# Kernel tuning notes

Hardware: AMD Instinct MI355X
Metric: run time of the kernel (lower is better)

## Reference

```python
import jax, jax.numpy as jnp
import numpy as np

B, N, H = 32, 256, 1024
HEADS, NHID = 8, 128
NCLS = 7
BAND = 24
ALPHA = 0.2          # GAT leaky-relu slope
NEG = -9e15          # masked-attention fill, as in pyGAT


def setup_inputs() -> dict:
    key = jax.random.key(0)
    ks = jax.random.split(key, 16)
    def nrm(k, shp, s=0.02):
        return jax.random.normal(k, shp, dtype=jnp.float32) * s
    hidden_cls = jax.random.normal(ks[0], (B, N, H), dtype=jnp.float32)
    hidden_emo = jax.random.normal(ks[1], (B, N, H), dtype=jnp.float32)
    # causal band cliques, diagonal included (GAT uses clique - eye)
    t = jnp.arange(N)
    band = ((t[None, :] <= t[:, None]) & (t[None, :] > t[:, None] - BAND)).astype(jnp.float32)
    clique = jnp.broadcast_to(band, (B, N, N))
    labels = jax.random.randint(ks[2], (B, N), 0, NCLS)
    pooler_W = nrm(ks[3], (H, H)); pooler_b = jnp.zeros((H,), jnp.float32)
    gat_W = nrm(ks[4], (HEADS, H, NHID))
    gat_a1 = nrm(ks[5], (HEADS, NHID)); gat_a2 = nrm(ks[6], (HEADS, NHID))
    out_W = nrm(ks[7], (H, H))            # heads*nhid == H -> nclass=H
    out_a1 = nrm(ks[8], (H,)); out_a2 = nrm(ks[9], (H,))
    lin1_W = nrm(ks[10], (H, H)); lin1_b = jnp.zeros((H,), jnp.float32)
    lin0_W = nrm(ks[11], (2 * H, H)); lin0_b = jnp.zeros((H,), jnp.float32)
    cls_W = nrm(ks[12], (H, NCLS)); cls_b = jnp.zeros((NCLS,), jnp.float32)
    A = jax.random.uniform(ks[13], (NCLS, NCLS), dtype=jnp.float32) + 0.1
    hmm_A = A / A.sum(axis=1, keepdims=True)   # row-stochastic transition matrix
    return dict(hidden_cls=hidden_cls, hidden_emo=hidden_emo, clique=clique,
                labels=labels, pooler_W=pooler_W, pooler_b=pooler_b,
                gat_W=gat_W, gat_a1=gat_a1, gat_a2=gat_a2,
                out_W=out_W, out_a1=out_a1, out_a2=out_a2,
                lin1_W=lin1_W, lin1_b=lin1_b, lin0_W=lin0_W, lin0_b=lin0_b,
                cls_W=cls_W, cls_b=cls_b, hmm_A=hmm_A)


def _lrelu(x):
    return jnp.where(x > 0, x, ALPHA * x)


def reference(hidden_cls, hidden_emo, clique, labels, pooler_W, pooler_b,
              gat_W, gat_a1, gat_a2, out_W, out_a1, out_a2,
              lin1_W, lin1_b, lin0_W, lin0_b, cls_W, cls_b, hmm_A):
    # PoolerAll: dense + tanh on all token states (dropout = identity in eval)
    fea_cls = jnp.tanh(hidden_cls @ pooler_W + pooler_b)   # [B,N,H] (CLS per utt)
    fea_emo = jnp.tanh(hidden_emo @ pooler_W + pooler_b)   # [B,N,H] (mask tok per utt)

    eyeN = jnp.eye(N, dtype=clique.dtype)
    adjm = (clique - eyeN) > 0                             # [B,N,N] GAT adjacency

    def gat_one(x, am):                                    # x [N,H], am [N,N]
        Wh = jnp.einsum('nf,hfd->hnd', x, gat_W)           # [heads,N,nhid]
        e = _lrelu(jnp.einsum('hnd,hd->hn', Wh, gat_a1)[:, :, None]
                   + jnp.einsum('hnd,hd->hn', Wh, gat_a2)[:, None, :])
        att = jax.nn.softmax(jnp.where(am[None], e, NEG), axis=-1)
        h1 = jax.nn.elu(jnp.einsum('hnm,hmd->hnd', att, Wh))
        h1 = jnp.transpose(h1, (1, 0, 2)).reshape(N, HEADS * NHID)
        Wh2 = h1 @ out_W                                   # out attention layer (concat=False)
        e2 = _lrelu((Wh2 @ out_a1)[:, None] + (Wh2 @ out_a2)[None, :])
        h2 = jax.nn.softmax(jnp.where(am, e2, NEG), axis=-1) @ Wh2
        return jax.nn.elu(h2)                              # [N,H]

    gat_out = jax.vmap(gat_one)(fea_cls, adjm)             # [B,N,H]
    # row 0 replaced by (dropout of) fea_cls row 0, as in the original
    g = jnp.concatenate([fea_cls[:, :1], gat_out[:, 1:]], axis=1)
    g = jnp.concatenate([fea_cls, g @ lin1_W + lin1_b], axis=-1) @ lin0_W + lin0_b
    log_gat = jax.nn.softmax(g @ cls_W + cls_b, axis=-1)   # [B,N,NCLS] (probs)

    # HMM emission probs hmm_B(fea) = softmax(classifier(fea))
    Bprob = jax.nn.softmax(fea_emo @ cls_W + cls_b, axis=-1)  # [B,N,NCLS]
    P0 = jnp.full((NCLS,), 1.0 / NCLS, dtype=jnp.float32)
    AT = hmm_A.T

    def hmm_row(Bp, mrow):                                 # Bp [N,NCLS], mrow [N]
        def step(carry, xs):
            p, started = carry
            bt, m = xs
            p_init = P0 * bt; p_init = p_init / p_init.sum()
            p_tr = (AT @ p) * bt; p_tr = p_tr / p_tr.sum()
            p_new = jnp.where(started, p_tr, p_init)
            valid = m > 0.5
            return (jnp.where(valid, p_new, p), started | valid), None
        (p, _), _ = jax.lax.scan(step, (P0, jnp.asarray(False)), (Bp, mrow))
        return p                                           # final filtered posterior

    log_hmm = jax.vmap(lambda Bp, M: jax.vmap(lambda mr: hmm_row(Bp, mr))(M))(Bprob, clique)

    logits = jnp.log((log_gat + log_hmm) * 0.5).reshape(B * N, NCLS)
    lab = labels.reshape(B * N)
    mask = lab >= 0
    picked = jnp.take_along_axis(logits, jnp.where(mask, lab, 0)[:, None], axis=1)[:, 0]
    loss = -(jnp.where(mask, picked, 0.0).sum() / jnp.maximum(mask.sum(), 1).astype(jnp.float32))
    return loss, logits
```

## Files before the change

### kernel.cpp

```cpp
#include <hip/hip_runtime.h>
#include <hip/hip_bf16.h>
#include <math.h>

typedef __hip_bfloat16 bf16;
typedef __attribute__((ext_vector_type(8))) short short8;
typedef __attribute__((ext_vector_type(4))) float float4v;

static constexpr int Bb = 32, Nn = 256, Hh = 1024, HEADS = 8, NHID = 128, NCLS = 7, BAND = 24;
static constexpr int M = Bb * Nn;
static constexpr float ALPHA = 0.2f;
static constexpr long INEL = (long)M * Hh;

__device__ __forceinline__ float tof(bf16 x) { return __bfloat162float(x); }
__device__ __forceinline__ bf16 tob(float x) { return __float2bfloat16(x); }
__device__ __forceinline__ unsigned short f2bits(float x) {
    bf16 h = __float2bfloat16(x);
    return *(unsigned short*)&h;
}
__device__ __forceinline__ float bits2f(unsigned short u) {
    unsigned v = ((unsigned)u) << 16;
    float f;
    __builtin_memcpy(&f, &v, 4);
    return f;
}

__device__ __forceinline__ void gload16(const void* g, void* l) {
    __builtin_amdgcn_global_load_lds(
        (const __attribute__((address_space(1))) void*)g,
        (__attribute__((address_space(3))) void*)l, 16, 0, 0);
}

static constexpr long OFF_PWT  = 0;
static constexpr long OFF_PB   = 1048576;
static constexpr long OFF_WCT  = 1049600;
static constexpr long OFF_GA1  = 2098176;
static constexpr long OFF_GA2  = 2099200;
static constexpr long OFF_OWT  = 2100224;
static constexpr long OFF_OA1  = 3148800;
static constexpr long OFF_OA2  = 3149824;
static constexpr long OFF_L1WT = 3150848;
static constexpr long OFF_L1B  = 4199424;
static constexpr long OFF_L0WT = 4200448;
static constexpr long OFF_L0B  = 6297600;
static constexpr long OFF_CWT  = 6298624;
static constexpr long OFF_CB   = 6305792;
static constexpr long OFF_HA   = 6305799;
static constexpr long W_TOTAL  = 6305848;

__global__ void probe_k(const void* __restrict__ p, int* __restrict__ flag) {
    int t = threadIdx.x;
    int bad = 0;
    for (int i = t; i < 4096; i += 256) {
        float v = tof(((const bf16*)p)[i]);
        if (!(fabsf(v) < 1e4f)) bad = 1;
    }
    __shared__ int sb[256];
    sb[t] = bad; __syncthreads();
    for (int s = 128; s; s >>= 1) { if (t < s) sb[t] |= sb[t + s]; __syncthreads(); }
    if (t == 0) *flag = sb[0] ? 0 : 1;
}

__device__ __forceinline__ float ldany(const void* p, long i, int isb) {
    return isb ? tof(((const bf16*)p)[i]) : ((const float*)p)[i];
}

__global__ void convert_k(const int* __restrict__ flagp,
                          const void* pW, const void* pb, const void* gW,
                          const void* ga1, const void* ga2, const void* oW,
                          const void* oa1, const void* oa2, const void* l1W,
                          const void* l1b, const void* l0W, const void* l0b,
                          const void* cW, const void* cb, const void* hA,
                          bf16* __restrict__ dst) {
    long idx = (long)blockIdx.x * 256 + threadIdx.x;
    if (idx >= W_TOTAL) return;
    int isb = *flagp;
    const void* src; long si;
    if      (idx < OFF_PB)   { long l = idx;            long n = l >> 10, k = l & 1023;
                               src = pW;  si = k * 1024 + n; }
    else if (idx < OFF_WCT)  { src = pb;  si = idx - OFF_PB; }
    else if (idx < OFF_GA1)  { long l = idx - OFF_WCT;  long n = l >> 10, f = l & 1023;
                               long h = n >> 7, d = n & 127;
                               src = gW;  si = h * 131072 + f * 128 + d; }
    else if (idx < OFF_GA2)  { src = ga1; si = idx - OFF_GA1; }
    else if (idx < OFF_OWT)  { src = ga2; si = idx - OFF_GA2; }
    else if (idx < OFF_OA1)  { long l = idx - OFF_OWT;  long n = l >> 10, k = l & 1023;
                               src = oW;  si = k * 1024 + n; }
    else if (idx < OFF_OA2)  { src = oa1; si = idx - OFF_OA1; }
    else if (idx < OFF_L1WT) { src = oa2; si = idx - OFF_OA2; }
    else if (idx < OFF_L1B)  { long l = idx - OFF_L1WT; long n = l >> 10, k = l & 1023;
                               src = l1W; si = k * 1024 + n; }
    else if (idx < OFF_L0WT) { src = l1b; si = idx - OFF_L1B; }
    else if (idx < OFF_L0B)  { long l = idx - OFF_L0WT; long n = l >> 11, k = l & 2047;
                               src = l0W; si = k * 1024 + n; }
    else if (idx < OFF_CWT)  { src = l0b; si = idx - OFF_L0B; }
    else if (idx < OFF_CB)   { long l = idx - OFF_CWT;  long c = l >> 10, k = l & 1023;
                               src = cW;  si = k * 7 + c; }
    else if (idx < OFF_HA)   { src = cb;  si = idx - OFF_CB; }
    else                     { src = hA;  si = idx - OFF_HA; }
    dst[idx] = tob(ldany(src, si, isb));
}

__global__ void convin_k(const int* __restrict__ flagp, const void* __restrict__ s0,
                         const void* __restrict__ s1, bf16* __restrict__ d0,
                         bf16* __restrict__ d1) {
    const int isb = *flagp;
    long i = ((long)blockIdx.x * 256 + threadIdx.x) * 8;
    const void* s; bf16* d; long off;
    if (i < INEL) { s = s0; d = d0; off = i; }
    else          { s = s1; d = d1; off = i - INEL; }
    if (isb) {
        *(int4*)(d + off) = *(const int4*)((const bf16*)s + off);
    } else {
        const float* f = (const float*)s + off;
        unsigned short tmp[8];
        #pragma unroll
        for (int q = 0; q < 8; ++q) tmp[q] = f2bits(f[q]);
        *(int4*)(d + off) = *(int4*)tmp;
    }
}

static constexpr int BUF_USHORT = 384 * 32;

template <int ACT>
__device__ __forceinline__ void gemm_pipe_core(
    const bf16* __restrict__ A0, const bf16* __restrict__ A1, int ksw,
    int strideA, const bf16* __restrict__ Bt, int strideB,
    const bf16* __restrict__ bias, bf16* __restrict__ Cout,
    int Nc, int K, int bm, int bn, unsigned short* lds) {
    const int tid = threadIdx.x;
    const int lane = tid & 63;
    const int wave = tid >> 6;
    const int wm = (wave >> 1) * 128;
    const int wn = (wave & 1) * 64;
    const int l15 = lane & 15, quad = lane >> 4;
    const int csw = ((lane & 3) ^ ((lane >> 2) & 3) ^ (lane >> 4)) * 8;
    const int sc8 = (quad ^ (l15 & 3) ^ (l15 >> 2)) * 8;

    long aoff[4], boff[2];
    #pragma unroll
    for (int o = 0; o < 4; ++o)
        aoff[o] = (long)(bm + wave * 64 + o * 16 + (lane >> 2)) * strideA + csw;
    #pragma unroll
    for (int o = 0; o < 2; ++o)
        boff[o] = (long)(bn + wave * 32 + o * 16 + (lane >> 2)) * strideB + csw;
    const int aDst = wave * 64 * 32;
    const int bDst = (256 + wave * 32) * 32;

    const int nt = K / 32;
    float4v acc[8][4];
    #pragma unroll
    for (int i = 0; i < 8; ++i)
        #pragma unroll
        for (int j = 0; j < 4; ++j) acc[i][j] = (float4v){0.f, 0.f, 0.f, 0.f};

    auto stage = [&](int ts, int bsel) {
        unsigned short* buf = lds + bsel * BUF_USHORT;
        int ksub = ts * 32;
        const bf16* Ap = A0; int ka = ksub;
        if (ksub >= ksw) { Ap = A1; ka = ksub - ksw; }
        #pragma unroll
        for (int o = 0; o < 4; ++o)
            gload16(Ap + aoff[o] + ka, buf + aDst + o * 512);
        #pragma unroll
        for (int o = 0; o < 2; ++o)
            gload16(Bt + boff[o] + ksub, buf + bDst + o * 512);
    };

    stage(0, 0);
    stage(1, 1);
    int cur = 0, nxt = 2;
    for (int t = 0; t < nt; ++t) {
        if (t < nt - 1) asm volatile("s_waitcnt vmcnt(6)" ::: "memory");
        else            asm volatile("s_waitcnt vmcnt(0)" ::: "memory");
        __builtin_amdgcn_s_barrier();
        asm volatile("" ::: "memory");
        if (t + 2 < nt) stage(t + 2, nxt);
        const unsigned short* bufc = lds + cur * BUF_USHORT;
        short8 af[8], bfr[4];
        #pragma unroll
        for (int j = 0; j < 4; ++j)
            bfr[j] = *(const short8*)(bufc + (256 + wn + j * 16 + l15) * 32 + sc8);
        #pragma unroll
        for (int i = 0; i < 8; ++i)
            af[i] = *(const short8*)(bufc + (wm + i * 16 + l15) * 32 + sc8);
        __builtin_amdgcn_s_setprio(1);
        #pragma unroll
        for (int i = 0; i < 8; ++i)
            #pragma unroll
            for (int j = 0; j < 4; ++j)
                acc[i][j] = __builtin_amdgcn_mfma_f32_16x16x32_bf16(bfr[j], af[i], acc[i][j], 0, 0, 0);
        __builtin_amdgcn_s_setprio(0);
        asm volatile("" ::: "memory");
        cur = cur == 2 ? 0 : cur + 1;
        nxt = nxt == 2 ? 0 : nxt + 1;
    }

    #pragma unroll
    for (int j = 0; j < 4; ++j) {
        int gn = bn + wn + j * 16 + quad * 4;
        float bj[4] = {0.f, 0.f, 0.f, 0.f};
        if (bias) {
            #pragma unroll
            for (int r = 0; r < 4; ++r) bj[r] = tof(bias[gn + r]);
        }
        #pragma unroll
        for (int i = 0; i < 8; ++i) {
            int gm = bm + wm + i * 16 + l15;
            float v0 = acc[i][j][0] + bj[0], v1 = acc[i][j][1] + bj[1];
            float v2 = acc[i][j][2] + bj[2], v3 = acc[i][j][3] + bj[3];
            if (ACT == 1) { v0 = tanhf(v0); v1 = tanhf(v1); v2 = tanhf(v2); v3 = tanhf(v3); }
            uint2 u;
            u.x = (unsigned)f2bits(v0) | ((unsigned)f2bits(v1) << 16);
            u.y = (unsigned)f2bits(v2) | ((unsigned)f2bits(v3) << 16);
            *(uint2*)(Cout + (long)gm * Nc + gn) = u;
        }
    }
}

template <int ACT>
__global__ __launch_bounds__(256, 2) void gemm_pipe_k(const bf16* __restrict__ A,
                                                      const bf16* __restrict__ Bt,
                                                      const bf16* __restrict__ bias,
                                                      bf16* __restrict__ Cout,
                                                      int Nc, int K) {
    __shared__ __align__(16) unsigned short lds[3 * BUF_USHORT];
    gemm_pipe_core<ACT>(A, A, K, K, Bt, K, bias, Cout, Nc, K,
                        blockIdx.x * 256, blockIdx.y * 128, lds);
}

__global__ __launch_bounds__(256, 2) void gemmP_pipe_k(const bf16* __restrict__ A0,
                                                       const bf16* __restrict__ A1,
                                                       const bf16* __restrict__ Bt,
                                                       const bf16* __restrict__ bias,
                                                       bf16* __restrict__ C0,
                                                       bf16* __restrict__ C1) {
    __shared__ __align__(16) unsigned short lds[3 * BUF_USHORT];
    const bf16* A = blockIdx.z ? A1 : A0;
    bf16* C = blockIdx.z ? C1 : C0;
    gemm_pipe_core<1>(A, A, Hh, Hh, Bt, Hh, bias, C, Hh, Hh,
                      blockIdx.x * 256, blockIdx.y * 128, lds);
}

__global__ __launch_bounds__(256, 2) void gemm2_pipe_k(const bf16* __restrict__ A0,
                                                       const bf16* __restrict__ A2,
                                                       const bf16* __restrict__ Bt,
                                                       const bf16* __restrict__ bias,
                                                       bf16* __restrict__ Cout) {
    __shared__ __align__(16) unsigned short lds[3 * BUF_USHORT];
    gemm_pipe_core<0>(A0, A2, 1024, 1024, Bt, 2048, bias, Cout, 1024, 2048,
                      blockIdx.x * 256, blockIdx.y * 128, lds);
}

__global__ __launch_bounds__(256) void att1f_k(const bf16* __restrict__ Wh,
                                               const bf16* __restrict__ ga1,
                                               const bf16* __restrict__ ga2,
                                               bf16* __restrict__ h1) {
    __shared__ unsigned short S[152][128];
    __shared__ float f1s[152], f2s[152];
    __shared__ float att[128][25];
    const int bx = blockIdx.x;
    const int b = bx >> 4, h = (bx >> 1) & 7, half = bx & 1;
    const int nbase = half * 128;
    const int mstart = half ? (nbase - (BAND - 1)) : 0;
    const int mcount = half ? (256 - mstart) : 128;
    const int t = threadIdx.x;
    const int c = t & 15;

    float av1[8], av2[8];
    {
        union { int4 v; unsigned short us[8]; } u1, u2;
        u1.v = *(const int4*)(ga1 + h * 128 + c * 8);
        u2.v = *(const int4*)(ga2 + h * 128 + c * 8);
        #pragma unroll
        for (int qq = 0; qq < 8; ++qq) { av1[qq] = bits2f(u1.us[qq]); av2[qq] = bits2f(u2.us[qq]); }
    }

    const int iters = (mcount * 16 + 255) >> 8;
    for (int i = 0; i < iters; ++i) {
        int li = i * 256 + t;
        int mr = li >> 4;
        if (mr < mcount) {
            long ga = (long)(b * 256 + mstart + mr) * 1024 + h * 128 + c * 8;
            union { int4 v; unsigned short us[8]; } u;
            u.v = *(const int4*)(Wh + ga);
            float p1 = 0.f, p2 = 0.f;
            #pragma unroll
            for (int qq = 0; qq < 8; ++qq) {
                float f = bits2f(u.us[qq]);
                p1 += f * av1[qq]; p2 += f * av2[qq];
            }
            *(int4*)&S[mr][c * 8] = u.v;
            #pragma unroll
            for (int mask = 1; mask < 16; mask <<= 1) {
                p1 += __shfl_xor(p1, mask);
                p2 += __shfl_xor(p2, mask);
            }
            if (c == 0) { f1s[mr] = p1; f2s[mr] = p2; }
        }
    }
    __syncthreads();

    if (t < 128) {
        int n = nbase + t;
        if (n > 0) {
            int cnt = n < (BAND - 1) ? n : (BAND - 1);
            int m0 = n - cnt;
            float f1n = f1s[n - mstart];
            float e[BAND - 1];
            float mx = -1e30f;
            for (int i = 0; i < cnt; ++i) {
                float v = f1n + f2s[m0 + i - mstart];
                v = v > 0.f ? v : ALPHA * v;
                e[i] = v; mx = fmaxf(mx, v);
            }
            float ss = 0.f;
            for (int i = 0; i < cnt; ++i) { e[i] = __expf(e[i] - mx); ss += e[i]; }
            float inv = 1.0f / ss;
            for (int i = 0; i < cnt; ++i) att[t][i] = e[i] * inv;
        }
    }
    __syncthreads();

    const int wave = t >> 6, lane = t & 63;
    for (int ln = wave; ln < 128; ln += 4) {
        int n = nbase + ln;
        if (n == 0) continue;
        int cnt = n < (BAND - 1) ? n : (BAND - 1);
        int mr0 = n - cnt - mstart;
        float s0 = 0.f, s1 = 0.f;
        for (int i = 0; i < cnt; ++i) {
            float a = att[ln][i];
            unsigned u = *(const unsigned*)&S[mr0 + i][lane * 2];
            s0 += a * bits2f((unsigned short)(u & 0xffff));
            s1 += a * bits2f((unsigned short)(u >> 16));
        }
        s0 = s0 > 0.f ? s0 : expm1f(s0);
        s1 = s1 > 0.f ? s1 : expm1f(s1);
        unsigned out = (unsigned)f2bits(s0) | ((unsigned)f2bits(s1) << 16);
        *(unsigned*)(h1 + (long)(b * 256 + n) * 1024 + h * 128 + lane * 2) = out;
    }
}

__global__ void mean1_k(const bf16* __restrict__ Wh, bf16* __restrict__ h1) {
    int bh = blockIdx.x;
    int h = bh & 7, b = bh >> 3;
    int lane = threadIdx.x;
    float s0 = 0.f, s1 = 0.f;
    long base = (long)(b * 256) * 1024 + h * 128 + lane * 2;
    for (int m = 0; m < 256; ++m) {
        unsigned u = *(const unsigned*)(Wh + base + (long)m * 1024);
        s0 += bits2f((unsigned short)(u & 0xffff));
        s1 += bits2f((unsigned short)(u >> 16));
    }
    s0 *= (1.0f / 256.0f); s1 *= (1.0f / 256.0f);
    s0 = s0 > 0.f ? s0 : expm1f(s0);
    s1 = s1 > 0.f ? s1 : expm1f(s1);
    unsigned out = (unsigned)f2bits(s0) | ((unsigned)f2bits(s1) << 16);
    *(unsigned*)(h1 + base) = out;
}

__global__ void f12b_k(const bf16* __restrict__ Wh2, const bf16* __restrict__ a1,
                       const bf16* __restrict__ a2, float* __restrict__ f1b,
                       float* __restrict__ f2b) {
    int idx = blockIdx.x;
    int lane = threadIdx.x;
    const bf16* row = Wh2 + (long)idx * 1024 + lane * 16;
    float s1 = 0.f, s2 = 0.f;
    #pragma unroll
    for (int half = 0; half < 2; ++half) {
        union { int4 v; unsigned short us[8]; } x, w1, w2;
        x.v  = *(const int4*)(row + half * 8);
        w1.v = *(const int4*)(a1 + lane * 16 + half * 8);
        w2.v = *(const int4*)(a2 + lane * 16 + half * 8);
        #pragma unroll
        for (int q = 0; q < 8; ++q) {
            float f = bits2f(x.us[q]);
            s1 += f * bits2f(w1.us[q]);
            s2 += f * bits2f(w2.us[q]);
        }
    }
    #pragma unroll
    for (int off = 32; off; off >>= 1) {
        s1 += __shfl_down(s1, off);
        s2 += __shfl_down(s2, off);
    }
    if (lane == 0) { f1b[idx] = s1; f2b[idx] = s2; }
}

__global__ __launch_bounds__(256) void att2f_k(const bf16* __restrict__ Wh2,
                                               const float* __restrict__ f1b,
                                               const float* __restrict__ f2b,
                                               bf16* __restrict__ g) {
    __shared__ unsigned short S[152][128];
    __shared__ float att[128][25];
    const int bx = blockIdx.x;
    const int b = bx >> 4, half = (bx >> 3) & 1, jt = bx & 7;
    const int nbase = half * 128;
    const int mstart = half ? (nbase - (BAND - 1)) : 0;
    const int mcount = half ? (256 - mstart) : 128;
    const int t = threadIdx.x;
    const int c = t & 15;

    const int iters = (mcount * 16 + 255) >> 8;
    for (int i = 0; i < iters; ++i) {
        int li = i * 256 + t;
        int mr = li >> 4;
        if (mr < mcount) {
            long ga = (long)(b * 256 + mstart + mr) * 1024 + jt * 128 + c * 8;
            *(int4*)&S[mr][c * 8] = *(const int4*)(Wh2 + ga);
        }
    }
    __syncthreads();

    if (t < 128) {
        int n = nbase + t;
        if (n > 0) {
            int cnt = n < (BAND - 1) ? n : (BAND - 1);
            int m0 = n - cnt;
            float f1n = f1b[b * 256 + n];
            float e[BAND - 1];
            float mx = -1e30f;
            for (int i = 0; i < cnt; ++i) {
                float v = f1n + f2b[b * 256 + m0 + i];
                v = v > 0.f ? v : ALPHA * v;
                e[i] = v; mx = fmaxf(mx, v);
            }
            float ss = 0.f;
            for (int i = 0; i < cnt; ++i) { e[i] = __expf(e[i] - mx); ss += e[i]; }
            float inv = 1.0f / ss;
            for (int i = 0; i < cnt; ++i) att[t][i] = e[i] * inv;
        }
    }
    __syncthreads();

    const int wave = t >> 6, lane = t & 63;
    for (int ln = wave; ln < 128; ln += 4) {
        int n = nbase + ln;
        if (n == 0) continue;
        int cnt = n < (BAND - 1) ? n : (BAND - 1);
        int mr0 = n - cnt - mstart;
        float s0 = 0.f, s1 = 0.f;
        for (int i = 0; i < cnt; ++i) {
            float a = att[ln][i];
            unsigned u = *(const unsigned*)&S[mr0 + i][lane * 2];
            s0 += a * bits2f((unsigned short)(u & 0xffff));
            s1 += a * bits2f((unsigned short)(u >> 16));
        }
        s0 = s0 > 0.f ? s0 : expm1f(s0);
        s1 = s1 > 0.f ? s1 : expm1f(s1);
        unsigned out = (unsigned)f2bits(s0) | ((unsigned)f2bits(s1) << 16);
        *(unsigned*)(g + (long)(b * 256 + n) * 1024 + jt * 128 + lane * 2) = out;
    }
}

__global__ void g_row0_k(const bf16* __restrict__ fea_cls, bf16* __restrict__ g) {
    int b = blockIdx.x;
    int t = threadIdx.x;
    long base = (long)(b * 256) * 1024 + t * 8;
    *(int4*)(g + base) = *(const int4*)(fea_cls + base);
}

__global__ void cls7_k(const bf16* __restrict__ X, const bf16* __restrict__ Wt,
                       const bf16* __restrict__ b, float* __restrict__ out, int K) {
    int row = blockIdx.x;
    int lane = threadIdx.x;
    float xv[16];
    {
        const bf16* x = X + (long)row * K + lane * 16;
        union { int4 v; unsigned short us[8]; } u0, u1;
        u0.v = *(const int4*)x; u1.v = *(const int4*)(x + 8);
        #pragma unroll
        for (int q = 0; q < 8; ++q) { xv[q] = bits2f(u0.us[q]); xv[q + 8] = bits2f(u1.us[q]); }
    }
    float acc[NCLS];
    #pragma unroll
    for (int cc = 0; cc < NCLS; ++cc) {
        const bf16* wr = Wt + (long)cc * K + lane * 16;
        union { int4 v; unsigned short us[8]; } w0, w1;
        w0.v = *(const int4*)wr; w1.v = *(const int4*)(wr + 8);
        float s = 0.f;
        #pragma unroll
        for (int q = 0; q < 8; ++q) {
            s += xv[q] * bits2f(w0.us[q]);
            s += xv[q + 8] * bits2f(w1.us[q]);
        }
        acc[cc] = s;
    }
    #pragma unroll
    for (int cc = 0; cc < NCLS; ++cc)
        #pragma unroll
        for (int off = 32; off; off >>= 1) acc[cc] += __shfl_down(acc[cc], off);
    if (lane == 0) {
        float mx = -1e30f;
        #pragma unroll
        for (int cc = 0; cc < NCLS; ++cc) { acc[cc] += tof(b[cc]); mx = fmaxf(mx, acc[cc]); }
        float s = 0.f;
        #pragma unroll
        for (int cc = 0; cc < NCLS; ++cc) { acc[cc] = expf(acc[cc] - mx); s += acc[cc]; }
        float inv = 1.0f / s;
        #pragma unroll
        for (int cc = 0; cc < NCLS; ++cc) out[(long)row * NCLS + cc] = acc[cc] * inv;
    }
}

__global__ void hmm_k(const float* __restrict__ Bprob, const bf16* __restrict__ hmm_A,
                      float* __restrict__ out) {
    __shared__ float AT[NCLS][NCLS];
    int t = threadIdx.x;
    if (t < NCLS * NCLS) {
        int i = t / NCLS, j = t % NCLS;
        AT[i][j] = tof(hmm_A[j * NCLS + i]);
    }
    __syncthreads();
    int idx = blockIdx.x * blockDim.x + t;
    int n = idx & 255, b = idx >> 8;
    int t0 = n - (BAND - 1) > 0 ? n - (BAND - 1) : 0;
    const float* Bp = Bprob + (long)(b * 256) * NCLS;
    float p[NCLS];
    float s = 0.f;
    #pragma unroll
    for (int cc = 0; cc < NCLS; ++cc) { p[cc] = Bp[t0 * NCLS + cc]; s += p[cc]; }
    float inv = 1.0f / s;
    #pragma unroll
    for (int cc = 0; cc < NCLS; ++cc) p[cc] *= inv;
    for (int tt = t0 + 1; tt <= n; ++tt) {
        float q[NCLS]; float ss = 0.f;
        #pragma unroll
        for (int i = 0; i < NCLS; ++i) {
            float a = 0.f;
            #pragma unroll
            for (int j = 0; j < NCLS; ++j) a += AT[i][j] * p[j];
            a *= Bp[tt * NCLS + i];
            q[i] = a; ss += a;
        }
        float iv = 1.0f / ss;
        #pragma unroll
        for (int i = 0; i < NCLS; ++i) p[i] = q[i] * iv;
    }
    #pragma unroll
    for (int cc = 0; cc < NCLS; ++cc) out[(long)idx * NCLS + cc] = p[cc];
}

__global__ void zero_k(float* p) { *p = 0.f; }

__global__ void final_k(const float* __restrict__ lg, const float* __restrict__ lh,
                        const int* __restrict__ labels, void* __restrict__ out,
                        float* __restrict__ loss_acc, const int* __restrict__ flagp) {
    int idx = blockIdx.x * blockDim.x + threadIdx.x;
    const int isb = *flagp;
    float lo[NCLS];
    int lab = labels[idx];
    #pragma unroll
    for (int c = 0; c < NCLS; ++c) {
        float v = logf(0.5f * (lg[(long)idx * NCLS + c] + lh[(long)idx * NCLS + c]));
        lo[c] = v;
        long o = 1 + (long)idx * NCLS + c;
        if (isb) ((bf16*)out)[o] = tob(v);
        else     ((float*)out)[o] = v;
    }
    float picked = lo[lab];
    __shared__ float red[256];
    red[threadIdx.x] = picked;
    __syncthreads();
    for (int s = 128; s; s >>= 1) {
        if (threadIdx.x < s) red[threadIdx.x] += red[threadIdx.x + s];
        __syncthreads();
    }
    if (threadIdx.x == 0) atomicAdd(loss_acc, red[0]);
}

__global__ void loss_k(const float* __restrict__ acc, void* __restrict__ out,
                       const int* __restrict__ flagp) {
    float v = -acc[0] / (float)(Bb * Nn);
    if (*flagp) ((bf16*)out)[0] = tob(v);
    else        ((float*)out)[0] = v;
}

extern "C" void kernel_launch(void* const* d_in, const int* in_sizes, int n_in,
                              void* d_out, int out_size, void* d_ws, size_t ws_size,
                              hipStream_t stream) {
    const void* hidden_cls = d_in[0];
    const void* hidden_emo = d_in[1];
    const int* labels = (const int*)d_in[3];

    char* w = (char*)d_ws;
    bf16* C  = (bf16*)w;
    bf16* E  = C + INEL;
    bf16* Wb = E + INEL;
    bf16* H2 = Wb + INEL;
    bf16* wc = H2 + INEL;
    float* f1b   = (float*)(wc + W_TOTAL);
    float* f2b   = f1b + M;
    float* Bprob = f2b + M;
    float* lgat  = Bprob + (long)M * NCLS;
    float* lhmm  = lgat + (long)M * NCLS;
    float* loss_acc = lhmm + (long)M * NCLS;
    int*   flag  = (int*)(loss_acc + 1);

    dim3 gblk(256);
    dim3 ggrid(M / 256, Hh / 128);
    dim3 pgrid(M / 256, Hh / 128, 2);

    probe_k<<<1, 256, 0, stream>>>(d_in[4], flag);
    convert_k<<<(int)((W_TOTAL + 255) / 256), 256, 0, stream>>>(
        flag, d_in[4], d_in[5], d_in[6], d_in[7], d_in[8], d_in[9], d_in[10],
        d_in[11], d_in[12], d_in[13], d_in[14], d_in[15], d_in[16], d_in[17],
        d_in[18], wc);
    convin_k<<<(int)(2 * INEL / (256 * 8)), 256, 0, stream>>>(flag, hidden_emo, hidden_cls, Wb, H2);

    gemmP_pipe_k<<<pgrid, gblk, 0, stream>>>(Wb, H2, wc + OFF_PWT, wc + OFF_PB, E, C);
    cls7_k<<<M, 64, 0, stream>>>(E, wc + OFF_CWT, wc + OFF_CB, Bprob, Hh);
    gemm_pipe_k<0><<<ggrid, gblk, 0, stream>>>(C, wc + OFF_WCT, (const bf16*)nullptr, Wb, Hh, Hh);
    att1f_k<<<512, 256, 0, stream>>>(Wb, wc + OFF_GA1, wc + OFF_GA2, E);
    mean1_k<<<Bb * HEADS, 64, 0, stream>>>(Wb, E);
    gemm_pipe_k<0><<<ggrid, gblk, 0, stream>>>(E, wc + OFF_OWT, (const bf16*)nullptr, Wb, Hh, Hh);
    f12b_k<<<M, 64, 0, stream>>>(Wb, wc + OFF_OA1, wc + OFF_OA2, f1b, f2b);
    g_row0_k<<<Bb, 128, 0, stream>>>(C, E);
    att2f_k<<<512, 256, 0, stream>>>(Wb, f1b, f2b, E);
    gemm_pipe_k<0><<<ggrid, gblk, 0, stream>>>(E, wc + OFF_L1WT, wc + OFF_L1B, Wb, Hh, Hh);
    gemm2_pipe_k<<<ggrid, gblk, 0, stream>>>(C, Wb, wc + OFF_L0WT, wc + OFF_L0B, E);
    cls7_k<<<M, 64, 0, stream>>>(E, wc + OFF_CWT, wc + OFF_CB, lgat, Hh);
    hmm_k<<<M / 256, 256, 0, stream>>>(Bprob, wc + OFF_HA, lhmm);
    zero_k<<<1, 1, 0, stream>>>(loss_acc);
    final_k<<<M / 256, 256, 0, stream>>>(lgat, lhmm, labels, d_out, loss_acc, flag);
    loss_k<<<1, 1, 0, stream>>>(loss_acc, d_out, flag);
}
```

Baseline: 495.2 us.

## Shrink GEMM tile to 128x128 with register double-buffered fragments and deeper prefetch

```diff
diff --git a/kernel.cpp b/kernel.cpp
--- a/kernel.cpp
+++ b/kernel.cpp
@@ -119,7 +119,7 @@
     }
 }
 
-static constexpr int BUF_USHORT = 384 * 32;
+static constexpr int SLOT_US = 256 * 32;
 
 template <int ACT>
 __device__ __forceinline__ void gemm_pipe_core(
@@ -130,125 +130,139 @@
     const int tid = threadIdx.x;
     const int lane = tid & 63;
     const int wave = tid >> 6;
-    const int wm = (wave >> 1) * 128;
-    const int wn = (wave & 1) * 64;
+    const int wm = (wave >> 1) * 64, wn = (wave & 1) * 64;
     const int l15 = lane & 15, quad = lane >> 4;
     const int csw = ((lane & 3) ^ ((lane >> 2) & 3) ^ (lane >> 4)) * 8;
     const int sc8 = (quad ^ (l15 & 3) ^ (l15 >> 2)) * 8;
 
-    long aoff[4], boff[2];
-    #pragma unroll
-    for (int o = 0; o < 4; ++o)
-        aoff[o] = (long)(bm + wave * 64 + o * 16 + (lane >> 2)) * strideA + csw;
-    #pragma unroll
-    for (int o = 0; o < 2; ++o)
+    long aoff[2], boff[2];
+    #pragma unroll
+    for (int o = 0; o < 2; ++o) {
+        aoff[o] = (long)(bm + wave * 32 + o * 16 + (lane >> 2)) * strideA + csw;
         boff[o] = (long)(bn + wave * 32 + o * 16 + (lane >> 2)) * strideB + csw;
-    const int aDst = wave * 64 * 32;
-    const int bDst = (256 + wave * 32) * 32;
+    }
+    const int aDst = wave * 32 * 32;
+    const int bDst = (128 + wave * 32) * 32;
 
     const int nt = K / 32;
-    float4v acc[8][4];
-    #pragma unroll
-    for (int i = 0; i < 8; ++i)
+    float4v acc[4][4];
+    #pragma unroll
+    for (int i = 0; i < 4; ++i)
         #pragma unroll
         for (int j = 0; j < 4; ++j) acc[i][j] = (float4v){0.f, 0.f, 0.f, 0.f};
 
-    auto stage = [&](int ts, int bsel) {
-        unsigned short* buf = lds + bsel * BUF_USHORT;
+    auto stage = [&](int ts, int slot) {
+        unsigned short* buf = lds + slot * SLOT_US;
         int ksub = ts * 32;
         const bf16* Ap = A0; int ka = ksub;
         if (ksub >= ksw) { Ap = A1; ka = ksub - ksw; }
-        #pragma unroll
-        for (int o = 0; o < 4; ++o)
-            gload16(Ap + aoff[o] + ka, buf + aDst + o * 512);
-        #pragma unroll
-        for (int o = 0; o < 2; ++o)
-            gload16(Bt + boff[o] + ksub, buf + bDst + o * 512);
+        gload16(Ap + aoff[0] + ka, buf + aDst);
+        gload16(Ap + aoff[1] + ka, buf + aDst + 512);
+        gload16(Bt + boff[0] + ksub, buf + bDst);
+        gload16(Bt + boff[1] + ksub, buf + bDst + 512);
     };
-
-    stage(0, 0);
-    stage(1, 1);
-    int cur = 0, nxt = 2;
-    for (int t = 0; t < nt; ++t) {
-        if (t < nt - 1) asm volatile("s_waitcnt vmcnt(6)" ::: "memory");
+    auto frags = [&](int slot, short8* af, short8* bfr) {
+        const unsigned short* bufc = lds + slot * SLOT_US;
+        #pragma unroll
+        for (int i = 0; i < 4; ++i)
+            af[i] = *(const short8*)(bufc + (wm + i * 16 + l15) * 32 + sc8);
+        #pragma unroll
+        for (int j = 0; j < 4; ++j)
+            bfr[j] = *(const short8*)(bufc + (128 + wn + j * 16 + l15) * 32 + sc8);
+    };
+
+    stage(0, 0); stage(1, 1); stage(2, 2);
+    asm volatile("s_waitcnt vmcnt(8)" ::: "memory");
+    __builtin_amdgcn_s_barrier();
+    asm volatile("" ::: "memory");
+    short8 afA[4], bfA[4], afB[4], bfB[4];
+    frags(0, afA, bfA);
+    int c0 = 0, c1 = 1, c2 = 2;
+
+    for (int t = 0; t < nt; t += 2) {
+        asm volatile("s_waitcnt lgkmcnt(0)" ::: "memory");
+        if (t < nt - 2) asm volatile("s_waitcnt vmcnt(4)" ::: "memory");
         else            asm volatile("s_waitcnt vmcnt(0)" ::: "memory");
         __builtin_amdgcn_s_barrier();
         asm volatile("" ::: "memory");
-        if (t + 2 < nt) stage(t + 2, nxt);
-        const unsigned short* bufc = lds + cur * BUF_USHORT;
-        short8 af[8], bfr[4];
-        #pragma unroll
-        for (int j = 0; j < 4; ++j)
-            bfr[j] = *(const short8*)(bufc + (256 + wn + j * 16 + l15) * 32 + sc8);
-        #pragma unroll
-        for (int i = 0; i < 8; ++i)
-            af[i] = *(const short8*)(bufc + (wm + i * 16 + l15) * 32 + sc8);
+        if (t + 3 < nt) stage(t + 3, c0);
+        if (t + 1 < nt) frags(c1, afB, bfB);
         __builtin_amdgcn_s_setprio(1);
         #pragma unroll
-        for (int i = 0; i < 8; ++i)
+        for (int i = 0; i < 4; ++i)
             #pragma unroll
             for (int j = 0; j < 4; ++j)
-                acc[i][j] = __builtin_amdgcn_mfma_f32_16x16x32_bf16(bfr[j], af[i], acc[i][j], 0, 0, 0);
+                acc[i][j] = __builtin_amdgcn_mfma_f32_16x16x32_bf16(afA[i], bfA[j], acc[i][j], 0, 0, 0);
         __builtin_amdgcn_s_setprio(0);
         asm volatile("" ::: "memory");
-        cur = cur == 2 ? 0 : cur + 1;
-        nxt = nxt == 2 ? 0 : nxt + 1;
+        asm volatile("s_waitcnt lgkmcnt(0)" ::: "memory");
+        if (t + 1 < nt - 2) asm volatile("s_waitcnt vmcnt(4)" ::: "memory");
+        else                asm volatile("s_waitcnt vmcnt(0)" ::: "memory");
+        __builtin_amdgcn_s_barrier();
+        asm volatile("" ::: "memory");
+        if (t + 4 < nt) stage(t + 4, c1);
+        if (t + 2 < nt) frags(c2, afA, bfA);
+        __builtin_amdgcn_s_setprio(1);
+        #pragma unroll
+        for (int i = 0; i < 4; ++i)
+            #pragma unroll
+            for (int j = 0; j < 4; ++j)
+                acc[i][j] = __builtin_amdgcn_mfma_f32_16x16x32_bf16(afB[i], bfB[j], acc[i][j], 0, 0, 0);
+        __builtin_amdgcn_s_setprio(0);
+        asm volatile("" ::: "memory");
+        int n0 = c2, n1 = c0, n2 = c1;
+        c0 = n0; c1 = n1; c2 = n2;
     }
 
     #pragma unroll
     for (int j = 0; j < 4; ++j) {
-        int gn = bn + wn + j * 16 + quad * 4;
-        float bj[4] = {0.f, 0.f, 0.f, 0.f};
-        if (bias) {
+        int gn = bn + wn + j * 16 + l15;
+        float bj = bias ? tof(bias[gn]) : 0.f;
+        #pragma unroll
+        for (int i = 0; i < 4; ++i) {
             #pragma unroll
-            for (int r = 0; r < 4; ++r) bj[r] = tof(bias[gn + r]);
-        }
-        #pragma unroll
-        for (int i = 0; i < 8; ++i) {
-            int gm = bm + wm + i * 16 + l15;
-            float v0 = acc[i][j][0] + bj[0], v1 = acc[i][j][1] + bj[1];
-            float v2 = acc[i][j][2] + bj[2], v3 = acc[i][j][3] + bj[3];
-            if (ACT == 1) { v0 = tanhf(v0); v1 = tanhf(v1); v2 = tanhf(v2); v3 = tanhf(v3); }
-            uint2 u;
-            u.x = (unsigned)f2bits(v0) | ((unsigned)f2bits(v1) << 16);
-            u.y = (unsigned)f2bits(v2) | ((unsigned)f2bits(v3) << 16);
-            *(uint2*)(Cout + (long)gm * Nc + gn) = u;
+            for (int r = 0; r < 4; ++r) {
+                int gm = bm + wm + i * 16 + quad * 4 + r;
+                float v = acc[i][j][r] + bj;
+                if (ACT == 1) v = tanhf(v);
+                Cout[(long)gm * Nc + gn] = tob(v);
+            }
         }
     }
 }
 
 template <int ACT>
-__global__ __launch_bounds__(256, 2) void gemm_pipe_k(const bf16* __restrict__ A,
+__global__ __launch_bounds__(256, 3) void gemm_pipe_k(const bf16* __restrict__ A,
                                                       const bf16* __restrict__ Bt,
                                                       const bf16* __restrict__ bias,
                                                       bf16* __restrict__ Cout,
                                                       int Nc, int K) {
-    __shared__ __align__(16) unsigned short lds[3 * BUF_USHORT];
+    __shared__ __align__(16) unsigned short lds[3 * SLOT_US];
     gemm_pipe_core<ACT>(A, A, K, K, Bt, K, bias, Cout, Nc, K,
-                        blockIdx.x * 256, blockIdx.y * 128, lds);
-}
-
-__global__ __launch_bounds__(256, 2) void gemmP_pipe_k(const bf16* __restrict__ A0,
+                        blockIdx.x * 128, blockIdx.y * 128, lds);
+}
+
+__global__ __launch_bounds__(256, 3) void gemmP_pipe_k(const bf16* __restrict__ A0,
                                                        const bf16* __restrict__ A1,
                                                        const bf16* __restrict__ Bt,
                                                        const bf16* __restrict__ bias,
                                                        bf16* __restrict__ C0,
                                                        bf16* __restrict__ C1) {
-    __shared__ __align__(16) unsigned short lds[3 * BUF_USHORT];
+    __shared__ __align__(16) unsigned short lds[3 * SLOT_US];
     const bf16* A = blockIdx.z ? A1 : A0;
     bf16* C = blockIdx.z ? C1 : C0;
     gemm_pipe_core<1>(A, A, Hh, Hh, Bt, Hh, bias, C, Hh, Hh,
-                      blockIdx.x * 256, blockIdx.y * 128, lds);
-}
-
-__global__ __launch_bounds__(256, 2) void gemm2_pipe_k(const bf16* __restrict__ A0,
+                      blockIdx.x * 128, blockIdx.y * 128, lds);
+}
+
+__global__ __launch_bounds__(256, 3) void gemm2_pipe_k(const bf16* __restrict__ A0,
                                                        const bf16* __restrict__ A2,
                                                        const bf16* __restrict__ Bt,
                                                        const bf16* __restrict__ bias,
                                                        bf16* __restrict__ Cout) {
-    __shared__ __align__(16) unsigned short lds[3 * BUF_USHORT];
+    __shared__ __align__(16) unsigned short lds[3 * SLOT_US];
     gemm_pipe_core<0>(A0, A2, 1024, 1024, Bt, 2048, bias, Cout, 1024, 2048,
-                      blockIdx.x * 256, blockIdx.y * 128, lds);
+                      blockIdx.x * 128, blockIdx.y * 128, lds);
 }
 
 __global__ __launch_bounds__(256) void att1f_k(const bf16* __restrict__ Wh,
@@ -598,8 +612,8 @@
     int*   flag  = (int*)(loss_acc + 1);
 
     dim3 gblk(256);
-    dim3 ggrid(M / 256, Hh / 128);
-    dim3 pgrid(M / 256, Hh / 128, 2);
+    dim3 ggrid(M / 128, Hh / 128);
+    dim3 pgrid(M / 128, Hh / 128, 2);
 
     probe_k<<<1, 256, 0, stream>>>(d_in[4], flag);
     convert_k<<<(int)((W_TOTAL + 255) / 256), 256, 0, stream>>>(
```

After: 481.5 us. -2.8%, faster.
